# Kernel optimization log

Measured on AMD Instinct MI355X. Metric: run time of the kernel, lower is better.

Reference implementation:

```python
import jax, jax.numpy as jnp
import numpy as np
from jax import lax

C_CLIP = 10.0
TEMP = 1.0
NEG = 1e8


def setup_inputs() -> dict:
    key = jax.random.key(0)
    ks = jax.random.split(key, 20)
    B, N, H, M = 16, 1000, 128, 2
    s = 0.08
    inp = {
        "enc_h": jax.random.normal(ks[0], (B, N, H), jnp.float32),
        "mask0": jnp.zeros((B, N), jnp.float32),
        "Wq1": jax.random.normal(ks[1], (M, 2 * H, H), jnp.float32) * s,
        "Wref1": jax.random.normal(ks[2], (M, H, H), jnp.float32) * s,
        "Vec1": jax.random.normal(ks[3], (M, H, H), jnp.float32) * s,
        "Wq3": jax.random.normal(ks[4], (M, H, H), jnp.float32) * s,
        "Wref3": jax.random.normal(ks[5], (M, H, H), jnp.float32) * s,
        "Vec3": jax.random.normal(ks[6], (M, H, H), jnp.float32) * s,
        "Wq4": jax.random.normal(ks[7], (M, H, H), jnp.float32) * s,
        "Wref4": jax.random.normal(ks[8], (M, H, H), jnp.float32) * s,
        "Vec4": jax.random.normal(ks[9], (M, H, H), jnp.float32) * s,
        "Wmh": jax.random.normal(ks[10], (M * H, H), jnp.float32) * s,
        "Wq2": jax.random.normal(ks[11], (H, H), jnp.float32) * s,
        "Wref2": jax.random.normal(ks[12], (H, H), jnp.float32) * s,
        "Vec2": jax.random.normal(ks[13], (H,), jnp.float32) * s,
        "dec_inp": jax.random.normal(ks[14], (H,), jnp.float32) * s,
        "n_decode": 16,
    }
    return inp


def reference(enc_h, mask0, Wq1, Wref1, Vec1, Wq3, Wref3, Vec3,
              Wq4, Wref4, Vec4, Wmh, Wq2, Wref2, Vec2, dec_inp, n_decode):
    B, N, H = enc_h.shape
    ref = enc_h
    h_mean = ref.mean(axis=1)  # [B,H] graph embedding (encoder mean)
    # Precompute per-head reference projections (hoisted out of decode loop)
    r1 = jnp.einsum('bnd,mdh->bmnh', ref, Wref1)
    v1 = jnp.einsum('bnd,mdh->bmnh', ref, Vec1)
    r3 = jnp.einsum('bnd,mdh->bmnh', ref, Wref3)
    v3 = jnp.einsum('bnd,mdh->bmnh', ref, Vec3)
    r4 = jnp.einsum('bnd,mdh->bmnh', ref, Wref4)
    v4 = jnp.einsum('bnd,mdh->bmnh', ref, Vec4)
    r2 = ref @ Wref2  # [B,N,H]

    def glimpse(query, Wq, r, v, mask):
        # query: [B,Din]; r,v: [B,M,N,H]; mask: [B,N] (1 = unavailable)
        q = jnp.einsum('bi,mih->bmh', query, Wq)
        u = jnp.tanh(q[:, :, None, :] + r)              # [B,M,N,H]
        s = jnp.einsum('bmnh,bmnh->bmn', u, v)          # additive scores
        s = C_CLIP * jnp.tanh(s)                        # logit clipping
        s = s - NEG * mask[:, None, :]
        a = jax.nn.softmax(s, axis=-1)                  # [B,M,N]
        g = jnp.einsum('bmn,bmnh->bmh', a, r)           # per-head glimpse
        return g.reshape(B, -1) @ Wmh                   # merge heads -> [B,H]

    def step(carry, _):
        mask, prev = carry
        q0 = jnp.concatenate([h_mean, prev], axis=-1)   # [B,2H]
        q = glimpse(q0, Wq1, r1, v1, mask)
        q = glimpse(q, Wq3, r3, v3, mask)
        q = glimpse(q, Wq4, r4, v4, mask)
        # pointer logits: Vec2 . tanh(W_q2 q + W_ref2 ref)
        u = jnp.einsum('h,bnh->bn', Vec2, jnp.tanh((q @ Wq2)[:, None, :] + r2))
        u = C_CLIP * jnp.tanh(u)
        u = u - NEG * mask
        logp = jax.nn.log_softmax(u / TEMP, axis=-1)    # [B,N]
        sel = jnp.argmax(logp, axis=-1)                 # greedy job selection
        mask = mask.at[jnp.arange(B), sel].set(1.0)
        prev = jnp.take_along_axis(ref, sel[:, None, None], axis=1)[:, 0]
        return (mask, prev), (logp, sel)

    prev0 = jnp.broadcast_to(dec_inp, (B, H))
    (_, _), (logps, sels) = lax.scan(step, (mask0, prev0), None, length=n_decode)
    return logps, sels
```

## Files before the change

kernel.cpp:

```cpp
#include <hip/hip_runtime.h>


#define Bb 16
#define Nn 1000
#define Hh 128
#define Ss 16
#define TPB 1024
#define NW 16
#define NB 16
#define ROWS 63
#define TPT (Nn * Bb * Hh)

#define PPART(par, g, c, m) \
  ((((size_t)(par)*16 + (size_t)(g))*NB + (size_t)(c))*2 + (size_t)(m))*132
#define ABUF(buf, g) (((size_t)(buf)*16 + (size_t)(g)) * 264)

typedef float f32x4 __attribute__((ext_vector_type(4)));
#define NTL(p) __builtin_nontemporal_load((const f32x4*)(p))

__device__ __forceinline__ void red5_2(float& a, float& b) {
#pragma unroll
  for (int m = 1; m <= 16; m <<= 1) {
    a += __shfl_xor(a, m, 64);
    b += __shfl_xor(b, m, 64);
  }
}
__device__ __forceinline__ void red5_4(float& a, float& b, float& c, float& d) {
#pragma unroll
  for (int m = 1; m <= 16; m <<= 1) {
    a += __shfl_xor(a, m, 64);
    b += __shfl_xor(b, m, 64);
    c += __shfl_xor(c, m, 64);
    d += __shfl_xor(d, m, 64);
  }
}

__device__ __forceinline__ float tanh_fast(float x) {
  const float xc = fminf(fmaxf(x, -10.f), 10.f);
  const float e = __expf(xc + xc);
  return (e - 1.f) * __builtin_amdgcn_rcpf(e + 1.f);
}
__device__ __forceinline__ float dot4t(const f32x4 q, const f32x4 r, const f32x4 v) {
  return tanh_fast(q[0] + r[0]) * v[0] + tanh_fast(q[1] + r[1]) * v[1] +
         tanh_fast(q[2] + r[2]) * v[2] + tanh_fast(q[3] + r[3]) * v[3];
}

__device__ __forceinline__ float aload(const float* p) {
  return __hip_atomic_load(p, __ATOMIC_RELAXED, __HIP_MEMORY_SCOPE_AGENT);
}
__device__ __forceinline__ void astore(float* p, float v) {
  __hip_atomic_store(p, v, __ATOMIC_RELAXED, __HIP_MEMORY_SCOPE_AGENT);
}

__device__ __forceinline__ void gbar(int* fl, int c, int p, int tid, int lane) {
  __syncthreads();
  if (tid < 64) {
    if (lane == 0)
      __hip_atomic_store(&fl[c * 32], p, __ATOMIC_RELEASE, __HIP_MEMORY_SCOPE_AGENT);
    int v = p;
    while (true) {
      if (lane < NB)
        v = __hip_atomic_load(&fl[lane * 32], __ATOMIC_RELAXED, __HIP_MEMORY_SCOPE_AGENT);
      if (__all(v >= p)) break;
      __builtin_amdgcn_s_sleep(1);
    }
  }
  __syncthreads();
}

__global__ __launch_bounds__(256) void ptr1_proj_kernel(
    const float* __restrict__ enc,
    const float* __restrict__ Wref1, const float* __restrict__ Vec1,
    const float* __restrict__ Wref3, const float* __restrict__ Vec3,
    const float* __restrict__ Wref4, const float* __restrict__ Vec4,
    const float* __restrict__ Wref2,
    float* __restrict__ outp) {
  __shared__ float At[128][64];
  __shared__ float Bs[128][64];
  const int rt = blockIdx.x;
  const int wy = blockIdx.y;
  const int mat = wy >> 1;
  const int ch = wy & 1;
  const int tid = threadIdx.x;

  const float* W;
  switch (mat >> 1) {
    case 0: W = Wref1; break;
    case 1: W = Vec1;  break;
    case 2: W = Wref3; break;
    case 3: W = Vec3;  break;
    case 4: W = Wref4; break;
    case 5: W = Vec4;  break;
    default: W = Wref2; break;
  }
  if (mat < 12) W += (size_t)(mat & 1) * (128 * 128);

  const float* asrc = enc + (size_t)rt * 64 * 128;
  for (int f = tid; f < 64 * 32; f += 256) {
    const int r = f >> 5, k4 = (f & 31) << 2;
    const float4 v = *(const float4*)(asrc + (size_t)r * 128 + k4);
    At[k4 + 0][r] = v.x; At[k4 + 1][r] = v.y;
    At[k4 + 2][r] = v.z; At[k4 + 3][r] = v.w;
  }
  for (int f = tid; f < 128 * 16; f += 256) {
    const int k = f >> 4, c4 = (f & 15) << 2;
    *(float4*)&Bs[k][c4] = *(const float4*)(W + (size_t)k * 128 + ch * 64 + c4);
  }
  __syncthreads();

  const int tx = tid & 15, ty = tid >> 4;
  float acc[4][4] = {{0.f}};
  for (int k = 0; k < 128; ++k) {
    const float4 a = *(const float4*)&At[k][ty * 4];
    const float4 b = *(const float4*)&Bs[k][tx * 4];
    acc[0][0] += a.x * b.x; acc[0][1] += a.x * b.y; acc[0][2] += a.x * b.z; acc[0][3] += a.x * b.w;
    acc[1][0] += a.y * b.x; acc[1][1] += a.y * b.y; acc[1][2] += a.y * b.z; acc[1][3] += a.y * b.w;
    acc[2][0] += a.z * b.x; acc[2][1] += a.z * b.y; acc[2][2] += a.z * b.z; acc[2][3] += a.z * b.w;
    acc[3][0] += a.w * b.x; acc[3][1] += a.w * b.y; acc[3][2] += a.w * b.z; acc[3][3] += a.w * b.w;
  }
  float* dst = outp + (size_t)mat * TPT + ((size_t)rt * 64 + ty * 4) * 128 + ch * 64 + tx * 4;
  for (int i = 0; i < 4; ++i) {
    float4 v; v.x = acc[i][0]; v.y = acc[i][1]; v.z = acc[i][2]; v.w = acc[i][3];
    *(float4*)(dst + (size_t)i * 128) = v;
  }
}

__global__ __launch_bounds__(1024, 4) void ptr1_decode_kernel(
    const float* __restrict__ enc, const float* __restrict__ mask0,
    const float* __restrict__ Wq1, const float* __restrict__ Wq3,
    const float* __restrict__ Wq4, const float* __restrict__ Wmh,
    const float* __restrict__ Wq2, const float* __restrict__ Vec2,
    const float* __restrict__ dec_inp, const float* __restrict__ proj,
    float* __restrict__ partials, float* __restrict__ accum,
    int* __restrict__ flags, float* __restrict__ out) {
  const int g = blockIdx.x >> 4;
  const int c = blockIdx.x & 15;
  const int tid = threadIdx.x;
  const int wv = tid >> 6;
  const int lane = tid & 63;
  const int half = lane >> 5;
  const int hl = lane & 31;
  const int h0 = hl << 2;
  const int start = c * ROWS;
  const int cnt = min(ROWS, Nn - start);
  const int jrow = wv * 2 + half;
  const int j2 = jrow + 32;
  const bool a2 = j2 < cnt;
  const int j2c = a2 ? j2 : jrow;
  int* fl = flags + g * (16 * 32);

  __shared__ float Wmh_lds[256 * 128];
  __shared__ __align__(16) float hmean[128];
  __shared__ __align__(16) float qprev[128];
  __shared__ __align__(16) float qcur[128];
  __shared__ __align__(16) float base1[256];
  __shared__ __align__(16) float qm[2][128];
  __shared__ __align__(16) float gfraw[256];
  __shared__ __align__(16) float vecl[128];
  __shared__ __align__(16) float wpart[NW][2][132];
  __shared__ __align__(16) float qpart[4][256];
  __shared__ __align__(16) float mpart[8][128];
  __shared__ float sS[2];
  __shared__ float maskl[64];
  __shared__ float ulocal[64];
  __shared__ int sel_sh;
  __shared__ float logZ_sh;

  {
    float4* wl = (float4*)Wmh_lds;
    const float4* wg = (const float4*)Wmh;
#pragma unroll
    for (int k = 0; k < 8; ++k) wl[tid + k * TPB] = wg[tid + k * TPB];
  }
  if (tid < 128) vecl[tid] = Vec2[tid];
  for (int j = tid; j < cnt; j += TPB) maskl[j] = mask0[(size_t)g * Nn + start + j];

  const size_t o1 = (size_t)jrow * Hh;
  const size_t o2 = (size_t)j2c * Hh;

  {
    const float* eb = enc + ((size_t)g * Nn + start) * Hh + h0;
    const float4 eA = *(const float4*)(eb + o1);
    const float4 eB = *(const float4*)(eb + o2);
    float4 a;
    a.x = eA.x + (a2 ? eB.x : 0.f); a.y = eA.y + (a2 ? eB.y : 0.f);
    a.z = eA.z + (a2 ? eB.z : 0.f); a.w = eA.w + (a2 ? eB.w : 0.f);
    a.x += __shfl_xor(a.x, 32, 64); a.y += __shfl_xor(a.y, 32, 64);
    a.z += __shfl_xor(a.z, 32, 64); a.w += __shfl_xor(a.w, 32, 64);
    if (half == 0) *(float4*)&wpart[wv][0][4 + h0] = a;
    __syncthreads();
    if (tid < 128) {
      float s = 0.f;
      for (int w = 0; w < NW; ++w) s += wpart[w][0][4 + tid];
      astore(&partials[PPART(0, g, c, 0) + 4 + tid], s);
    }
    gbar(fl, c, 1, tid, lane);
    if (tid < 128) {
      float s = 0.f;
#pragma unroll 8
      for (int cc = 0; cc < NB; ++cc) s += aload(&partials[PPART(0, g, cc, 0) + 4 + tid]);
      hmean[tid] = s * (1.0f / (float)Nn);
    }
    if (tid >= 128 && tid < 256) qprev[tid - 128] = dec_inp[tid - 128];
    __syncthreads();
    {
      const int o = tid & 255, part = tid >> 8;
      const int m = o >> 7, h = o & 127;
      const float* wp = Wq1 + (size_t)m * 256 * 128 + (size_t)(part * 32) * 128 + h;
      const float* qc = hmean + part * 32;
      float acc = 0.f;
#pragma unroll 16
      for (int i = 0; i < 32; ++i) acc += qc[i] * wp[(size_t)i * 128];
      qpart[part][o] = acc;
    }
    __syncthreads();
    if (tid < 256)
      base1[tid] = qpart[0][tid] + qpart[1][tid] + qpart[2][tid] + qpart[3][tid];
    __syncthreads();
  }

  int p = 2;
  for (int step = 0; step < Ss; ++step) {
    for (int gl = 0; gl < 3; ++gl) {
      const size_t rowb = ((size_t)g * Nn + start) * Hh + h0;
      const float* r0p = proj + (size_t)(4 * gl + 0) * TPT + rowb;
      const float* r1p = proj + (size_t)(4 * gl + 1) * TPT + rowb;
      const float* v0p = proj + (size_t)(4 * gl + 2) * TPT + rowb;
      const float* v1p = proj + (size_t)(4 * gl + 3) * TPT + rowb;
      const f32x4 r0A = NTL(r0p + o1), r0B = NTL(r0p + o2);
      const f32x4 r1A = NTL(r1p + o1), r1B = NTL(r1p + o2);
      const f32x4 v0A = NTL(v0p + o1), v0B = NTL(v0p + o2);
      const f32x4 v1A = NTL(v1p + o1), v1B = NTL(v1p + o2);
      {
        const int o = tid & 255, part = tid >> 8;
        const int m = o >> 7, h = o & 127;
        const float* wp;
        const float* qc;
        if (gl == 0) {
          wp = Wq1 + (size_t)m * 256 * 128 + (size_t)(128 + part * 32) * 128 + h;
          qc = qprev + part * 32;
        } else {
          const float* Wq = (gl == 1) ? Wq3 : Wq4;
          wp = Wq + (size_t)m * 128 * 128 + (size_t)(part * 32) * 128 + h;
          qc = qcur + part * 32;
        }
        float acc = 0.f;
#pragma unroll 16
        for (int i = 0; i < 32; ++i) acc += qc[i] * wp[(size_t)i * 128];
        qpart[part][o] = acc;
      }
      __syncthreads();
      if (tid < 256) {
        float s = qpart[0][tid] + qpart[1][tid] + qpart[2][tid] + qpart[3][tid];
        if (gl == 0) s += base1[tid];
        (&qm[0][0])[tid] = s;
      }
      __syncthreads();

      const f32x4 qa = *(const f32x4*)&qm[0][h0];
      const f32x4 qb = *(const f32x4*)&qm[1][h0];
      const float mlA = maskl[jrow], mlB = maskl[j2c];
      float s0A = dot4t(qa, r0A, v0A), s1A = dot4t(qb, r1A, v1A);
      float s0B = dot4t(qa, r0B, v0B), s1B = dot4t(qb, r1B, v1B);
      red5_4(s0A, s1A, s0B, s1B);
      s0A = 10.f * tanh_fast(s0A) - 1e8f * mlA;
      s1A = 10.f * tanh_fast(s1A) - 1e8f * mlA;
      s0B = 10.f * tanh_fast(s0B) - 1e8f * mlB;
      s1B = 10.f * tanh_fast(s1B) - 1e8f * mlB;
      const float e0A = __expf(s0A - 10.f), e1A = __expf(s1A - 10.f);
      const float e0B = a2 ? __expf(s0B - 10.f) : 0.f;
      const float e1B = a2 ? __expf(s1B - 10.f) : 0.f;
      float S0 = e0A + e0B, S1 = e1A + e1B;
      float4 g0, g1;
      g0.x = e0A * r0A[0] + e0B * r0B[0]; g0.y = e0A * r0A[1] + e0B * r0B[1];
      g0.z = e0A * r0A[2] + e0B * r0B[2]; g0.w = e0A * r0A[3] + e0B * r0B[3];
      g1.x = e1A * r1A[0] + e1B * r1B[0]; g1.y = e1A * r1A[1] + e1B * r1B[1];
      g1.z = e1A * r1A[2] + e1B * r1B[2]; g1.w = e1A * r1A[3] + e1B * r1B[3];
      S0 += __shfl_xor(S0, 32, 64); S1 += __shfl_xor(S1, 32, 64);
      g0.x += __shfl_xor(g0.x, 32, 64); g0.y += __shfl_xor(g0.y, 32, 64);
      g0.z += __shfl_xor(g0.z, 32, 64); g0.w += __shfl_xor(g0.w, 32, 64);
      g1.x += __shfl_xor(g1.x, 32, 64); g1.y += __shfl_xor(g1.y, 32, 64);
      g1.z += __shfl_xor(g1.z, 32, 64); g1.w += __shfl_xor(g1.w, 32, 64);
      if (half == 0) {
        *(float4*)&wpart[wv][0][4 + h0] = g0;
        *(float4*)&wpart[wv][1][4 + h0] = g1;
        if (hl == 0) { wpart[wv][0][0] = S0; wpart[wv][1][0] = S1; }
      }
      __syncthreads();
      float* ab = accum + ABUF(p & 3, g);
      float* zb = accum + ABUF((p + 1) & 3, g);
      if (tid < 256) {
        const int m = tid >> 7, h = tid & 127;
        float gs = 0.f;
        for (int w = 0; w < NW; ++w) gs += wpart[w][m][4 + h];
        unsafeAtomicAdd(&ab[m * 132 + 4 + h], gs);
        if (h == 0) {
          float ss = 0.f;
          for (int w = 0; w < NW; ++w) ss += wpart[w][m][0];
          unsafeAtomicAdd(&ab[m * 132], ss);
        }
      } else if (tid >= 512 && tid < 512 + 17) {
        const int idx = c * 17 + (tid - 512);
        if (idx < 264) astore(&zb[idx], 0.f);
      }
      gbar(fl, c, p, tid, lane);
      p++;
      if (tid < 256) gfraw[tid] = aload(&ab[(tid >> 7) * 132 + 4 + (tid & 127)]);
      if (tid >= 256 && tid < 258) sS[tid - 256] = aload(&ab[(tid - 256) * 132]);
      __syncthreads();
      {
        const int h = tid & 127, part = tid >> 7;
        const int m = part >> 2;
        float acc = 0.f;
        const float* wl = Wmh_lds + (size_t)part * 32 * 128 + h;
        const float* gg = gfraw + part * 32;
#pragma unroll 16
        for (int i = 0; i < 32; ++i) acc += gg[i] * wl[i * 128];
        mpart[part][h] = acc / sS[m];
      }
      __syncthreads();
      if (tid < 128) {
        float acc = 0.f;
        for (int w = 0; w < 8; ++w) acc += mpart[w][tid];
        qcur[tid] = acc;
      }
      __syncthreads();
    }

    const float* r2p = proj + (size_t)12 * TPT + ((size_t)g * Nn + start) * Hh + h0;
    const f32x4 rrA = NTL(r2p + o1);
    const f32x4 rrB = NTL(r2p + o2);
    {
      const int h = tid & 127, part = tid >> 7;
      float acc = 0.f;
      const float* wp = Wq2 + (size_t)part * 16 * 128 + h;
      const float* qc = qcur + part * 16;
#pragma unroll
      for (int i = 0; i < 16; ++i) acc += qc[i] * wp[(size_t)i * 128];
      mpart[part][h] = acc;
    }
    __syncthreads();
    if (tid < 128) {
      float acc = 0.f;
      for (int w = 0; w < 8; ++w) acc += mpart[w][tid];
      qm[0][tid] = acc;
    }
    __syncthreads();
    {
      const f32x4 q2 = *(const f32x4*)&qm[0][h0];
      const f32x4 vz = *(const f32x4*)&vecl[h0];
      float upA = dot4t(q2, rrA, vz);
      float upB = dot4t(q2, rrB, vz);
      red5_2(upA, upB);
      const float mlA = maskl[jrow], mlB = maskl[j2c];
      const float uA = 10.f * tanh_fast(upA) - 1e8f * mlA;
      const float uB = a2 ? (10.f * tanh_fast(upB) - 1e8f * mlB) : -3.0e38f;
      if (hl == 0) {
        ulocal[jrow] = uA;
        if (a2) ulocal[j2] = uB;
      }
      float Sv = __expf(uA - 10.f) + (a2 ? __expf(uB - 10.f) : 0.f);
      float um = uA; int ui = start + jrow;
      if (a2 && uB > um) { um = uB; ui = start + j2; }
      Sv += __shfl_xor(Sv, 32, 64);
      const float um2 = __shfl_xor(um, 32, 64);
      const int ui2 = __shfl_xor(ui, 32, 64);
      if (um2 > um || (um2 == um && ui2 < ui)) { um = um2; ui = ui2; }
      if (lane == 0) {
        wpart[wv][0][0] = Sv; wpart[wv][0][1] = um;
        wpart[wv][0][2] = __int_as_float(ui);
      }
    }
    __syncthreads();
    const int par = p & 1;
    if (tid == 0) {
      float St = 0.f, bm = -3.0e38f; int bi = 0x7fffffff;
      for (int ww = 0; ww < NW; ++ww) {
        St += wpart[ww][0][0];
        const float m2 = wpart[ww][0][1];
        const int i2 = __float_as_int(wpart[ww][0][2]);
        if (m2 > bm || (m2 == bm && i2 < bi)) { bm = m2; bi = i2; }
      }
      float* gp = partials + PPART(par, g, c, 0);
      astore(&gp[0], St); astore(&gp[1], bm);
      astore(&gp[2], __int_as_float(bi));
    } else if (tid >= 512 && tid < 512 + 17) {
      float* zb = accum + ABUF((p + 1) & 3, g);
      const int idx = c * 17 + (tid - 512);
      if (idx < 264) astore(&zb[idx], 0.f);
    }
    gbar(fl, c, p, tid, lane);
    p++;
    if (tid < 64) {
      float St = 0.f, bm = -3.0e38f; int bi = 0x7fffffff;
      if (lane < NB) {
        const float* gp = partials + PPART(par, g, lane, 0);
        St = aload(&gp[0]); bm = aload(&gp[1]);
        bi = __float_as_int(aload(&gp[2]));
      }
#pragma unroll
      for (int m2 = 1; m2 <= 8; m2 <<= 1) {
        St += __shfl_xor(St, m2, 64);
        const float bm2 = __shfl_xor(bm, m2, 64);
        const int bi2 = __shfl_xor(bi, m2, 64);
        if (bm2 > bm || (bm2 == bm && bi2 < bi)) { bm = bm2; bi = bi2; }
      }
      if (lane == 0) { sel_sh = bi; logZ_sh = 10.f + __logf(St); }
    }
    __syncthreads();
    const int sel = sel_sh;
    const float lz = logZ_sh;
    if (tid < 128)
      qprev[tid] = enc[((size_t)g * Nn + sel) * Hh + tid];
    for (int j = tid; j < cnt; j += TPB)
      out[(size_t)step * (Bb * Nn) + (size_t)g * Nn + start + j] = ulocal[j] - lz;
    if (c == 0 && tid == 0)
      out[(size_t)Ss * Bb * Nn + (size_t)step * Bb + g] = (float)sel;
    if (tid == 0 && sel >= start && sel < start + cnt) maskl[sel - start] = 1.0f;
    __syncthreads();
  }
}

extern "C" void kernel_launch(void* const* d_in, const int* in_sizes, int n_in,
                              void* d_out, int out_size, void* d_ws, size_t ws_size,
                              hipStream_t stream) {
  const float* enc     = (const float*)d_in[0];
  const float* mask0   = (const float*)d_in[1];
  const float* Wq1     = (const float*)d_in[2];
  const float* Wref1   = (const float*)d_in[3];
  const float* Vec1    = (const float*)d_in[4];
  const float* Wq3     = (const float*)d_in[5];
  const float* Wref3   = (const float*)d_in[6];
  const float* Vec3    = (const float*)d_in[7];
  const float* Wq4     = (const float*)d_in[8];
  const float* Wref4   = (const float*)d_in[9];
  const float* Vec4    = (const float*)d_in[10];
  const float* Wmh     = (const float*)d_in[11];
  const float* Wq2     = (const float*)d_in[12];
  const float* Wref2   = (const float*)d_in[13];
  const float* Vec2    = (const float*)d_in[14];
  const float* dec_inp = (const float*)d_in[15];
  float* out = (float*)d_out;

  char* ws = (char*)d_ws;
  int* flags      = (int*)ws;
  float* accum    = (float*)(ws + 32768);
  float* partials = (float*)(ws + 102400);
  float* proj     = (float*)(ws + 102400 + 540672);

  hipMemsetAsync(ws, 0, 102400, stream);

  dim3 pg(250, 26);
  ptr1_proj_kernel<<<pg, 256, 0, stream>>>(enc, Wref1, Vec1, Wref3, Vec3,
                                           Wref4, Vec4, Wref2, proj);

  void* args[] = {(void*)&enc,  (void*)&mask0, (void*)&Wq1, (void*)&Wq3,
                  (void*)&Wq4,  (void*)&Wmh,   (void*)&Wq2, (void*)&Vec2,
                  (void*)&dec_inp, (void*)&proj, (void*)&partials,
                  (void*)&accum, (void*)&flags, (void*)&out};
  hipLaunchCooperativeKernel((const void*)ptr1_decode_kernel, dim3(256),
                             dim3(1024), args, 0, stream);
}
```

Baseline: 1.002 ms.

## Replace partials exchange with packed atomic argmax and drop barrier spin sleep

```diff
diff --git a/kernel.cpp b/kernel.cpp
--- a/kernel.cpp
+++ b/kernel.cpp
@@ -13,7 +13,7 @@
 
 #define PPART(par, g, c, m) \
   ((((size_t)(par)*16 + (size_t)(g))*NB + (size_t)(c))*2 + (size_t)(m))*132
-#define ABUF(buf, g) (((size_t)(buf)*16 + (size_t)(g)) * 264)
+#define ABUF(buf, g) (((size_t)(buf)*16 + (size_t)(g)) * 272)
 
 typedef float f32x4 __attribute__((ext_vector_type(4)));
 #define NTL(p) __builtin_nontemporal_load((const f32x4*)(p))
@@ -62,7 +62,6 @@
       if (lane < NB)
         v = __hip_atomic_load(&fl[lane * 32], __ATOMIC_RELAXED, __HIP_MEMORY_SCOPE_AGENT);
       if (__all(v >= p)) break;
-      __builtin_amdgcn_s_sleep(1);
     }
   }
   __syncthreads();
@@ -231,6 +230,7 @@
       const f32x4 r1A = NTL(r1p + o1), r1B = NTL(r1p + o2);
       const f32x4 v0A = NTL(v0p + o1), v0B = NTL(v0p + o2);
       const f32x4 v1A = NTL(v1p + o1), v1B = NTL(v1p + o2);
+      __builtin_amdgcn_sched_barrier(0);
       {
         const int o = tid & 255, part = tid >> 8;
         const int m = o >> 7, h = o & 127;
@@ -301,7 +301,7 @@
         }
       } else if (tid >= 512 && tid < 512 + 17) {
         const int idx = c * 17 + (tid - 512);
-        if (idx < 264) astore(&zb[idx], 0.f);
+        if (idx < 272) astore(&zb[idx], 0.f);
       }
       gbar(fl, c, p, tid, lane);
       p++;
@@ -330,6 +330,7 @@
     const float* r2p = proj + (size_t)12 * TPT + ((size_t)g * Nn + start) * Hh + h0;
     const f32x4 rrA = NTL(r2p + o1);
     const f32x4 rrB = NTL(r2p + o2);
+    __builtin_amdgcn_sched_barrier(0);
     {
       const int h = tid & 127, part = tid >> 7;
       float acc = 0.f;
@@ -372,7 +373,8 @@
       }
     }
     __syncthreads();
-    const int par = p & 1;
+    float* ab = accum + ABUF(p & 3, g);
+    float* zb = accum + ABUF((p + 1) & 3, g);
     if (tid == 0) {
       float St = 0.f, bm = -3.0e38f; int bi = 0x7fffffff;
       for (int ww = 0; ww < NW; ++ww) {
@@ -381,31 +383,25 @@
         const int i2 = __float_as_int(wpart[ww][0][2]);
         if (m2 > bm || (m2 == bm && i2 < bi)) { bm = m2; bi = i2; }
       }
-      float* gp = partials + PPART(par, g, c, 0);
-      astore(&gp[0], St); astore(&gp[1], bm);
-      astore(&gp[2], __int_as_float(bi));
+      unsigned ob = __float_as_uint(bm);
+      ob = (ob & 0x80000000u) ? ~ob : (ob | 0x80000000u);
+      const unsigned long long key =
+          ((unsigned long long)ob << 32) | (0xFFFFFFFFu - (unsigned)bi);
+      unsafeAtomicAdd(&ab[0], St);
+      atomicMax((unsigned long long*)&ab[264], key);
     } else if (tid >= 512 && tid < 512 + 17) {
-      float* zb = accum + ABUF((p + 1) & 3, g);
       const int idx = c * 17 + (tid - 512);
-      if (idx < 264) astore(&zb[idx], 0.f);
+      if (idx < 272) astore(&zb[idx], 0.f);
     }
     gbar(fl, c, p, tid, lane);
     p++;
-    if (tid < 64) {
-      float St = 0.f, bm = -3.0e38f; int bi = 0x7fffffff;
-      if (lane < NB) {
-        const float* gp = partials + PPART(par, g, lane, 0);
-        St = aload(&gp[0]); bm = aload(&gp[1]);
-        bi = __float_as_int(aload(&gp[2]));
-      }
-#pragma unroll
-      for (int m2 = 1; m2 <= 8; m2 <<= 1) {
-        St += __shfl_xor(St, m2, 64);
-        const float bm2 = __shfl_xor(bm, m2, 64);
-        const int bi2 = __shfl_xor(bi, m2, 64);
-        if (bm2 > bm || (bm2 == bm && bi2 < bi)) { bm = bm2; bi = bi2; }
-      }
-      if (lane == 0) { sel_sh = bi; logZ_sh = 10.f + __logf(St); }
+    if (tid == 0) {
+      const float St = aload(&ab[0]);
+      const unsigned long long key = __hip_atomic_load(
+          (const unsigned long long*)&ab[264], __ATOMIC_RELAXED,
+          __HIP_MEMORY_SCOPE_AGENT);
+      sel_sh = (int)(0xFFFFFFFFu - (unsigned)(key & 0xFFFFFFFFu));
+      logZ_sh = 10.f + __logf(St);
     }
     __syncthreads();
     const int sel = sel_sh;
```

New measurement: 993.9 us (median of 2 runs). No clear change (-0.8%).
